# Kernel tuning notes

Hardware: AMD Instinct MI355X
Metric: run time of the kernel (lower is better)

Reference implementation:

```python
import jax, jax.numpy as jnp
import numpy as np

B, S, D = 4, 2048, 512
H, DK, DV = 8, 64, 64


def setup_inputs() -> dict:
    key = jax.random.key(0)
    ks = jax.random.split(key, 12)
    inv = 1.0 / np.sqrt(D)
    return {
        "query": jax.random.normal(ks[0], (B, S, D), dtype=jnp.float32),
        "value": jax.random.normal(ks[1], (B, S, D), dtype=jnp.float32),
        "attention_mask": jax.random.randint(ks[2], (B, S), 0, 2, dtype=jnp.int32),
        "Wq": jax.random.normal(ks[3], (D, H * DK), dtype=jnp.float32) * inv,
        "bq": jnp.zeros((H * DK,), dtype=jnp.float32),
        "Wk": jax.random.normal(ks[4], (D, H * DK), dtype=jnp.float32) * inv,
        "bk": jnp.zeros((H * DK,), dtype=jnp.float32),
        "Wv": jax.random.normal(ks[5], (D, H * DV), dtype=jnp.float32) * inv,
        "bv": jnp.zeros((H * DV,), dtype=jnp.float32),
        "Wo": jax.random.normal(ks[6], (H * DV, D), dtype=jnp.float32) * inv,
        "bo": jnp.zeros((D,), dtype=jnp.float32),
    }


def _split_heads(x, h):
    b, s, _ = x.shape
    return x.reshape(b, s, h, -1).transpose(0, 2, 1, 3)  # (B,H,S,dh)


def reference(query, value, attention_mask, Wq, bq, Wk, bk, Wv, bv, Wo, bo):
    # QKV projections (activation=None -> identity); key defaults to value
    q = _split_heads(query @ Wq + bq, H)   # (B,H,S,DK)
    k = _split_heads(value @ Wk + bk, H)   # (B,H,S,DK)
    v = _split_heads(value @ Wv + bv, H)   # (B,H,S,DV)

    scores = jnp.einsum("bhqd,bhkd->bhqk", q, k) / jnp.sqrt(jnp.float32(DK))
    # additive mask: m = 1e9*(mask-1), applied on both key and query axes
    m = 1e9 * (attention_mask.astype(jnp.float32) - 1.0)  # (B,S)
    scores = scores + m[:, None, None, :] + m[:, None, :, None]

    weights = jax.nn.softmax(scores, axis=-1)
    ctx = jnp.einsum("bhqk,bhkd->bhqd", weights, v)        # (B,H,S,DV)
    ctx = ctx.transpose(0, 2, 1, 3).reshape(ctx.shape[0], ctx.shape[2], H * DV)
    return ctx @ Wo + bo  # (B,S,D)
```

## Files before the change

### kernel.cpp

```cpp
#include <hip/hip_runtime.h>

#define B_ 4
#define S_ 2048
#define D_ 512
#define H_ 8

typedef __attribute__((ext_vector_type(8))) __bf16 bf16x8;
typedef __attribute__((ext_vector_type(4))) float f32x4;

#define NEGBIG  -1.442695040e9f
#define QSCALE  0.18033688011112042f

__device__ __forceinline__ unsigned pack_rn(float a, float b) {
    union { float f; unsigned u; } ua, ub; ua.f = a; ub.f = b;
    return __builtin_amdgcn_perm(ub.u + 0x8000u, ua.u + 0x8000u, 0x07060302u);
}

__global__ __launch_bounds__(256) void cast_x(
    const float* __restrict__ q, const float* __restrict__ v,
    unsigned short* __restrict__ xq, unsigned short* __restrict__ xv)
{
    const float* src = blockIdx.z ? v : q;
    unsigned short* dst = blockIdx.z ? xv : xq;
    int i = (blockIdx.x * 256 + threadIdx.x) * 8;
    float4 f0 = *(const float4*)&src[i];
    float4 f1 = *(const float4*)&src[i + 4];
    uint4 o;
    o.x = pack_rn(f0.x, f0.y); o.y = pack_rn(f0.z, f0.w);
    o.z = pack_rn(f1.x, f1.y); o.w = pack_rn(f1.z, f1.w);
    *(uint4*)&dst[i] = o;
}

__global__ __launch_bounds__(256) void cast_wt(
    const float* __restrict__ Wq, const float* __restrict__ Wk,
    const float* __restrict__ Wv, const float* __restrict__ Wo,
    unsigned short* __restrict__ Tq, unsigned short* __restrict__ Tk,
    unsigned short* __restrict__ Tv, unsigned short* __restrict__ To)
{
    int z = blockIdx.z;
    const float* W = (z == 0) ? Wq : (z == 1) ? Wk : (z == 2) ? Wv : Wo;
    unsigned short* T = (z == 0) ? Tq : (z == 1) ? Tk : (z == 2) ? Tv : To;
    int n0 = blockIdx.x * 64, k0 = blockIdx.y * 64;
    int tid = threadIdx.x;

    __shared__ float Ts[64][69];
    #pragma unroll
    for (int it = 0; it < 4; it++) {
        int lin = tid + it * 256;
        int kr = lin >> 4, c4 = (lin & 15) * 4;
        float4 v = *(const float4*)&W[(k0 + kr) * 512 + n0 + c4];
        Ts[kr][c4 + 0] = v.x; Ts[kr][c4 + 1] = v.y;
        Ts[kr][c4 + 2] = v.z; Ts[kr][c4 + 3] = v.w;
    }
    __syncthreads();
    int n = tid >> 2, kc = tid & 3;
    unsigned p[8];
    #pragma unroll
    for (int j = 0; j < 8; j++)
        p[j] = pack_rn(Ts[kc * 16 + 2 * j][n], Ts[kc * 16 + 2 * j + 1][n]);
    unsigned short* dst = &T[(n0 + n) * 512 + k0 + kc * 16];
    *(uint4*)dst       = *(uint4*)&p[0];
    *(uint4*)(dst + 8) = *(uint4*)&p[4];
}

__global__ __launch_bounds__(256) void proj_qkv_mfma(
    const unsigned short* __restrict__ Xq, const unsigned short* __restrict__ Xv,
    const unsigned short* __restrict__ Wtq, const unsigned short* __restrict__ Wtk,
    const unsigned short* __restrict__ Wtv,
    const float* __restrict__ bq, const float* __restrict__ bk,
    const float* __restrict__ bv,
    unsigned short* __restrict__ Qb, unsigned short* __restrict__ Kb,
    unsigned short* __restrict__ VtG)
{
    const int z = blockIdx.z;
    const unsigned short* A  = (z == 0) ? Wtq : (z == 1) ? Wtk : Xv;
    const unsigned short* Bm = (z == 0) ? Xq  : (z == 1) ? Xv  : Wtv;
    const float* bias        = (z == 0) ? bq  : (z == 1) ? bk  : bv;
    const int m0 = (z < 2) ? blockIdx.y * 128 : blockIdx.x * 128;
    const int n0 = (z < 2) ? blockIdx.x * 128 : blockIdx.y * 128;

    const int tid = threadIdx.x;
    const int w = tid >> 6, lane = tid & 63;
    const int l15 = lane & 15, quad = lane >> 4;
    const int wm = (w >> 1) * 64, wn = (w & 1) * 64;

    __shared__ unsigned short As[128 * 72];
    __shared__ unsigned short Bs[128 * 72];

    f32x4 acc[4][4];
    #pragma unroll
    for (int i = 0; i < 4; i++)
        #pragma unroll
        for (int j = 0; j < 4; j++) acc[i][j] = (f32x4){0.f, 0.f, 0.f, 0.f};

    for (int k0 = 0; k0 < 512; k0 += 64) {
        __syncthreads();
        #pragma unroll
        for (int it = 0; it < 2; it++) {
            int lin = tid + it * 256;
            int row = lin >> 2, c2 = (lin & 3) * 2;
            *(uint4*)&As[row * 72 + c2 * 8]     = *(const uint4*)&A[(m0 + row) * 512 + k0 + c2 * 8];
            *(uint4*)&As[row * 72 + c2 * 8 + 8] = *(const uint4*)&A[(m0 + row) * 512 + k0 + c2 * 8 + 8];
            *(uint4*)&Bs[row * 72 + c2 * 8]     = *(const uint4*)&Bm[(n0 + row) * 512 + k0 + c2 * 8];
            *(uint4*)&Bs[row * 72 + c2 * 8 + 8] = *(const uint4*)&Bm[(n0 + row) * 512 + k0 + c2 * 8 + 8];
        }
        __syncthreads();
        #pragma unroll
        for (int kc = 0; kc < 2; kc++) {
            bf16x8 a[4], bb[4];
            #pragma unroll
            for (int i = 0; i < 4; i++)
                a[i] = *(const bf16x8*)&As[(wm + 16 * i + l15) * 72 + kc * 32 + quad * 8];
            #pragma unroll
            for (int j = 0; j < 4; j++)
                bb[j] = *(const bf16x8*)&Bs[(wn + 16 * j + l15) * 72 + kc * 32 + quad * 8];
            #pragma unroll
            for (int i = 0; i < 4; i++)
                #pragma unroll
                for (int j = 0; j < 4; j++)
                    acc[i][j] = __builtin_amdgcn_mfma_f32_16x16x32_bf16(a[i], bb[j], acc[i][j], 0, 0, 0);
        }
    }

    if (z == 2) {
        #pragma unroll
        for (int j = 0; j < 4; j++) {
            int N = n0 + wn + 16 * j + l15;
            float bv_ = bias[N];
            int h = N >> 6, d = N & 63;
            #pragma unroll
            for (int i = 0; i < 4; i++) {
                int Mb = m0 + wm + 16 * i + quad * 4;
                int b = Mb >> 11, s = Mb & 2047;
                uint2 o;
                o.x = pack_rn(acc[i][j][0] + bv_, acc[i][j][1] + bv_);
                o.y = pack_rn(acc[i][j][2] + bv_, acc[i][j][3] + bv_);
                *(uint2*)&VtG[((b * H_ + h) * 64 + d) * 2048 + s] = o;
            }
        }
    } else {
        unsigned short* dst = (z == 0) ? Qb : Kb;
        const float scale = (z == 0) ? QSCALE : 1.0f;
        #pragma unroll
        for (int j = 0; j < 4; j++) {
            int sg = n0 + wn + 16 * j + l15;
            int b = sg >> 11, s = sg & 2047;
            #pragma unroll
            for (int i = 0; i < 4; i++) {
                int F = m0 + wm + 16 * i + quad * 4;
                int h = F >> 6, d = F & 63;
                float4 b4 = *(const float4*)&bias[F];
                uint2 o;
                o.x = pack_rn((acc[i][j][0] + b4.x) * scale, (acc[i][j][1] + b4.y) * scale);
                o.y = pack_rn((acc[i][j][2] + b4.z) * scale, (acc[i][j][3] + b4.w) * scale);
                *(uint2*)&dst[((b * H_ + h) * 2048 + s) * 64 + d] = o;
            }
        }
    }
}

__global__ __launch_bounds__(256) void flash_mfma(
    const unsigned short* __restrict__ Qg, const unsigned short* __restrict__ Kg,
    const unsigned short* __restrict__ VtG, const int* __restrict__ amask,
    unsigned short* __restrict__ ctxB)
{
    const int bh = blockIdx.y, b = bh >> 3, h = bh & 7;
    const int q0 = blockIdx.x * 128;
    const int tid = threadIdx.x;
    const int w = tid >> 6, lane = tid & 63;
    const int l15 = lane & 15, quad = lane >> 4;

    __shared__ unsigned short Ks[2][64 * 72];
    __shared__ unsigned short Ps[4][32 * 72];
    __shared__ float Km[4][64];

    const int* amask_b = amask + b * 2048;
    unsigned short* pw = &Ps[w][0];

    bf16x8 qf[2][2];
    float mq[2];
    #pragma unroll
    for (int qb = 0; qb < 2; qb++) {
        int qrow = q0 + w * 32 + qb * 16 + l15;
        const unsigned short* p = &Qg[(bh * 2048 + qrow) * 64 + quad * 8];
        qf[qb][0] = *(const bf16x8*)p;
        qf[qb][1] = *(const bf16x8*)(p + 32);
        mq[qb] = amask_b[qrow] ? 0.f : NEGBIG;
    }

    const int srow = tid >> 2;
    const int sch  = (tid & 3) * 2;
    const unsigned short* kgb = Kg + (long)bh * 2048 * 64;

    {
        uint4 k0a = *(const uint4*)&kgb[srow * 64 + sch * 8];
        uint4 k0b = *(const uint4*)&kgb[srow * 64 + sch * 8 + 8];
        *(uint4*)&Ks[0][srow * 72 + sch * 8]     = k0a;
        *(uint4*)&Ks[0][srow * 72 + sch * 8 + 8] = k0b;
    }
    int mreg = amask_b[lane];

    f32x4 accO[2][4];
    #pragma unroll
    for (int qb = 0; qb < 2; qb++)
        #pragma unroll
        for (int dt = 0; dt < 4; dt++) accO[qb][dt] = (f32x4){0.f, 0.f, 0.f, 0.f};
    float mi[2] = {-3.0e38f, -3.0e38f};
    float li[2] = {0.f, 0.f};

    __syncthreads();

    for (int t = 0; t < 32; t++) {
        const int kt = t * 64;
        const int ktn = (t < 31) ? kt + 64 : kt;
        const int cur = t & 1, nxt = cur ^ 1;

        bf16x8 vf[4][2];
        #pragma unroll
        for (int dt = 0; dt < 4; dt++)
            #pragma unroll
            for (int kc = 0; kc < 2; kc++)
                vf[dt][kc] = *(const bf16x8*)&VtG[(bh * 64 + dt * 16 + l15) * 2048 + kt + kc * 32 + quad * 8];
        uint4 kst0 = *(const uint4*)&kgb[(ktn + srow) * 64 + sch * 8];
        uint4 kst1 = *(const uint4*)&kgb[(ktn + srow) * 64 + sch * 8 + 8];
        Km[w][lane] = mreg ? 0.f : NEGBIG;
        mreg = amask_b[ktn + lane];

        f32x4 kmf[4];
        #pragma unroll
        for (int nt = 0; nt < 4; nt++)
            kmf[nt] = *(const f32x4*)&Km[w][nt * 16 + quad * 4];

        bf16x8 kf[4][2];
        #pragma unroll
        for (int nt = 0; nt < 4; nt++)
            #pragma unroll
            for (int kc = 0; kc < 2; kc++)
                kf[nt][kc] = *(const bf16x8*)&Ks[cur][(nt * 16 + l15) * 72 + kc * 32 + quad * 8];
        f32x4 sc[2][4];
        #pragma unroll
        for (int qb = 0; qb < 2; qb++)
            #pragma unroll
            for (int nt = 0; nt < 4; nt++) {
                sc[qb][nt] = kmf[nt] + mq[qb];
                #pragma unroll
                for (int kc = 0; kc < 2; kc++)
                    sc[qb][nt] = __builtin_amdgcn_mfma_f32_16x16x32_bf16(
                        kf[nt][kc], qf[qb][kc], sc[qb][nt], 0, 0, 0);
            }

        #pragma unroll
        for (int qb = 0; qb < 2; qb++) {
            float mloc = sc[qb][0][0];
            #pragma unroll
            for (int nt = 0; nt < 4; nt++)
                #pragma unroll
                for (int r = 0; r < 4; r++)
                    mloc = fmaxf(mloc, sc[qb][nt][r]);
            mloc = fmaxf(mloc, __shfl_xor(mloc, 16));
            mloc = fmaxf(mloc, __shfl_xor(mloc, 32));
            float mn = fmaxf(mi[qb], mloc);
            float alpha = __builtin_amdgcn_exp2f(mi[qb] - mn);
            float ps = 0.f;
            #pragma unroll
            for (int nt = 0; nt < 4; nt++) {
                float p0 = __builtin_amdgcn_exp2f(sc[qb][nt][0] - mn);
                float p1 = __builtin_amdgcn_exp2f(sc[qb][nt][1] - mn);
                float p2 = __builtin_amdgcn_exp2f(sc[qb][nt][2] - mn);
                float p3 = __builtin_amdgcn_exp2f(sc[qb][nt][3] - mn);
                ps += (p0 + p1) + (p2 + p3);
                int prow = (qb * 16 + l15) * 72 + nt * 16 + quad * 4;
                *(unsigned*)&pw[prow]     = pack_rn(p0, p1);
                *(unsigned*)&pw[prow + 2] = pack_rn(p2, p3);
            }
            ps += __shfl_xor(ps, 16);
            ps += __shfl_xor(ps, 32);
            li[qb] = li[qb] * alpha + ps;
            mi[qb] = mn;
            #pragma unroll
            for (int dt = 0; dt < 4; dt++) {
                accO[qb][dt][0] *= alpha; accO[qb][dt][1] *= alpha;
                accO[qb][dt][2] *= alpha; accO[qb][dt][3] *= alpha;
            }
        }

        #pragma unroll
        for (int qb = 0; qb < 2; qb++) {
            bf16x8 pf0 = *(const bf16x8*)&pw[(qb * 16 + l15) * 72 + quad * 8];
            bf16x8 pf1 = *(const bf16x8*)&pw[(qb * 16 + l15) * 72 + 32 + quad * 8];
            #pragma unroll
            for (int dt = 0; dt < 4; dt++) {
                accO[qb][dt] = __builtin_amdgcn_mfma_f32_16x16x32_bf16(
                    vf[dt][0], pf0, accO[qb][dt], 0, 0, 0);
                accO[qb][dt] = __builtin_amdgcn_mfma_f32_16x16x32_bf16(
                    vf[dt][1], pf1, accO[qb][dt], 0, 0, 0);
            }
        }

        *(uint4*)&Ks[nxt][srow * 72 + sch * 8]     = kst0;
        *(uint4*)&Ks[nxt][srow * 72 + sch * 8 + 8] = kst1;
        __syncthreads();
    }

    #pragma unroll
    for (int qb = 0; qb < 2; qb++) {
        float inv = 1.f / li[qb];
        int q = q0 + w * 32 + qb * 16 + l15;
        int obase = (b * 2048 + q) * 512 + h * 64 + quad * 4;
        #pragma unroll
        for (int dt = 0; dt < 4; dt++) {
            uint2 o;
            o.x = pack_rn(accO[qb][dt][0] * inv, accO[qb][dt][1] * inv);
            o.y = pack_rn(accO[qb][dt][2] * inv, accO[qb][dt][3] * inv);
            *(uint2*)&ctxB[obase + dt * 16] = o;
        }
    }
}

__global__ __launch_bounds__(256) void proj_out_mfma(
    const unsigned short* __restrict__ ctxB, const unsigned short* __restrict__ Wto,
    const float* __restrict__ bo, float* __restrict__ out)
{
    const int m0 = blockIdx.y * 128, n0 = blockIdx.x * 128;
    const int tid = threadIdx.x;
    const int w = tid >> 6, lane = tid & 63;
    const int l15 = lane & 15, quad = lane >> 4;
    const int wm = (w >> 1) * 64, wn = (w & 1) * 64;

    __shared__ unsigned short As[128 * 72];
    __shared__ unsigned short Bs[128 * 72];

    f32x4 acc[4][4];
    #pragma unroll
    for (int i = 0; i < 4; i++)
        #pragma unroll
        for (int j = 0; j < 4; j++) acc[i][j] = (f32x4){0.f, 0.f, 0.f, 0.f};

    for (int k0 = 0; k0 < 512; k0 += 64) {
        __syncthreads();
        #pragma unroll
        for (int it = 0; it < 2; it++) {
            int lin = tid + it * 256;
            int row = lin >> 2, c2 = (lin & 3) * 2;
            *(uint4*)&As[row * 72 + c2 * 8]     = *(const uint4*)&Wto[(m0 + row) * 512 + k0 + c2 * 8];
            *(uint4*)&As[row * 72 + c2 * 8 + 8] = *(const uint4*)&Wto[(m0 + row) * 512 + k0 + c2 * 8 + 8];
            *(uint4*)&Bs[row * 72 + c2 * 8]     = *(const uint4*)&ctxB[(n0 + row) * 512 + k0 + c2 * 8];
            *(uint4*)&Bs[row * 72 + c2 * 8 + 8] = *(const uint4*)&ctxB[(n0 + row) * 512 + k0 + c2 * 8 + 8];
        }
        __syncthreads();
        #pragma unroll
        for (int kc = 0; kc < 2; kc++) {
            bf16x8 a[4], bb[4];
            #pragma unroll
            for (int i = 0; i < 4; i++)
                a[i] = *(const bf16x8*)&As[(wm + 16 * i + l15) * 72 + kc * 32 + quad * 8];
            #pragma unroll
            for (int j = 0; j < 4; j++)
                bb[j] = *(const bf16x8*)&Bs[(wn + 16 * j + l15) * 72 + kc * 32 + quad * 8];
            #pragma unroll
            for (int i = 0; i < 4; i++)
                #pragma unroll
                for (int j = 0; j < 4; j++)
                    acc[i][j] = __builtin_amdgcn_mfma_f32_16x16x32_bf16(a[i], bb[j], acc[i][j], 0, 0, 0);
        }
    }

    #pragma unroll
    for (int j = 0; j < 4; j++) {
        int sg = n0 + wn + 16 * j + l15;
        #pragma unroll
        for (int i = 0; i < 4; i++) {
            int F = m0 + wm + 16 * i + quad * 4;
            float4 b4 = *(const float4*)&bo[F];
            float4 vv;
            vv.x = acc[i][j][0] + b4.x;
            vv.y = acc[i][j][1] + b4.y;
            vv.z = acc[i][j][2] + b4.z;
            vv.w = acc[i][j][3] + b4.w;
            *(float4*)&out[sg * 512 + F] = vv;
        }
    }
}

extern "C" void kernel_launch(void* const* d_in, const int* in_sizes, int n_in,
                              void* d_out, int out_size, void* d_ws, size_t ws_size,
                              hipStream_t stream)
{
    const float* query = (const float*)d_in[0];
    const float* value = (const float*)d_in[1];
    const int*   amask = (const int*)d_in[2];
    const float* Wq = (const float*)d_in[3];
    const float* bq = (const float*)d_in[4];
    const float* Wk = (const float*)d_in[5];
    const float* bk = (const float*)d_in[6];
    const float* Wv = (const float*)d_in[7];
    const float* bv = (const float*)d_in[8];
    const float* Wo = (const float*)d_in[9];
    const float* bo = (const float*)d_in[10];
    float* out = (float*)d_out;

    char* ws = (char*)d_ws;
    const size_t MB = 1 << 20;
    unsigned short* Xbq = (unsigned short*)(ws);
    unsigned short* Xbv = (unsigned short*)(ws + 8 * MB);
    unsigned short* Wtq = (unsigned short*)(ws + 16 * MB);
    unsigned short* Wtk = (unsigned short*)(ws + 16 * MB + MB / 2);
    unsigned short* Wtv = (unsigned short*)(ws + 17 * MB);
    unsigned short* Wto = (unsigned short*)(ws + 17 * MB + MB / 2);
    unsigned short* Qb  = (unsigned short*)(ws + 18 * MB);
    unsigned short* Kb  = (unsigned short*)(ws + 26 * MB);
    unsigned short* VtG = (unsigned short*)(ws + 34 * MB);
    unsigned short* ctx = (unsigned short*)(ws + 42 * MB);

    cast_x<<<dim3(2048, 1, 2), 256, 0, stream>>>(query, value, Xbq, Xbv);
    cast_wt<<<dim3(8, 8, 4), 256, 0, stream>>>(Wq, Wk, Wv, Wo, Wtq, Wtk, Wtv, Wto);
    proj_qkv_mfma<<<dim3(64, 4, 3), 256, 0, stream>>>(Xbq, Xbv, Wtq, Wtk, Wtv,
                                                      bq, bk, bv, Qb, Kb, VtG);
    flash_mfma<<<dim3(16, 32), 256, 0, stream>>>(Qb, Kb, VtG, amask, ctx);
    proj_out_mfma<<<dim3(64, 4), 256, 0, stream>>>(ctx, Wto, bo, out);
}
```

Baseline: 214.8 us.

## Halve flash query tile and stage V tiles through double-buffered LDS

The flash attention kernel now gives each block 64 query rows instead of 128, with one 16-row block per wave, and doubles the grid to 1024 blocks with a launch bound asking for 4 blocks per CU. V tiles are now loaded cooperatively into a double-buffered shared-memory buffer alongside K, where before each wave read them directly from global memory into registers. The aim is more blocks and lower register pressure for better latency hiding, plus coalesced V loads. The cost is that every K/V tile is now fetched twice as often across the grid, and each wave does less MFMA work per tile load and barrier.

```diff
diff --git a/kernel.cpp b/kernel.cpp
--- a/kernel.cpp
+++ b/kernel.cpp
@@ -159,54 +159,50 @@
     }
 }
 
-__global__ __launch_bounds__(256) void flash_mfma(
+__global__ __launch_bounds__(256, 4) void flash_mfma(
     const unsigned short* __restrict__ Qg, const unsigned short* __restrict__ Kg,
     const unsigned short* __restrict__ VtG, const int* __restrict__ amask,
     unsigned short* __restrict__ ctxB)
 {
     const int bh = blockIdx.y, b = bh >> 3, h = bh & 7;
-    const int q0 = blockIdx.x * 128;
+    const int q0 = blockIdx.x * 64;
     const int tid = threadIdx.x;
     const int w = tid >> 6, lane = tid & 63;
     const int l15 = lane & 15, quad = lane >> 4;
 
     __shared__ unsigned short Ks[2][64 * 72];
-    __shared__ unsigned short Ps[4][32 * 72];
+    __shared__ unsigned short Vs[2][64 * 72];
+    __shared__ unsigned short Ps[4][16 * 72];
     __shared__ float Km[4][64];
 
     const int* amask_b = amask + b * 2048;
     unsigned short* pw = &Ps[w][0];
 
-    bf16x8 qf[2][2];
-    float mq[2];
-    #pragma unroll
-    for (int qb = 0; qb < 2; qb++) {
-        int qrow = q0 + w * 32 + qb * 16 + l15;
+    const int qrow = q0 + w * 16 + l15;
+    bf16x8 qf[2];
+    {
         const unsigned short* p = &Qg[(bh * 2048 + qrow) * 64 + quad * 8];
-        qf[qb][0] = *(const bf16x8*)p;
-        qf[qb][1] = *(const bf16x8*)(p + 32);
-        mq[qb] = amask_b[qrow] ? 0.f : NEGBIG;
-    }
+        qf[0] = *(const bf16x8*)p;
+        qf[1] = *(const bf16x8*)(p + 32);
+    }
+    const float mq = amask_b[qrow] ? 0.f : NEGBIG;
 
     const int srow = tid >> 2;
     const int sch  = (tid & 3) * 2;
-    const unsigned short* kgb = Kg + (long)bh * 2048 * 64;
-
-    {
-        uint4 k0a = *(const uint4*)&kgb[srow * 64 + sch * 8];
-        uint4 k0b = *(const uint4*)&kgb[srow * 64 + sch * 8 + 8];
-        *(uint4*)&Ks[0][srow * 72 + sch * 8]     = k0a;
-        *(uint4*)&Ks[0][srow * 72 + sch * 8 + 8] = k0b;
-    }
+    const unsigned short* kgb = Kg  + (long)bh * 2048 * 64;
+    const unsigned short* vgb = VtG + (long)bh * 64 * 2048;
+
+    *(uint4*)&Ks[0][srow * 72 + sch * 8]     = *(const uint4*)&kgb[srow * 64 + sch * 8];
+    *(uint4*)&Ks[0][srow * 72 + sch * 8 + 8] = *(const uint4*)&kgb[srow * 64 + sch * 8 + 8];
+    *(uint4*)&Vs[0][srow * 72 + sch * 8]     = *(const uint4*)&vgb[srow * 2048 + sch * 8];
+    *(uint4*)&Vs[0][srow * 72 + sch * 8 + 8] = *(const uint4*)&vgb[srow * 2048 + sch * 8 + 8];
     int mreg = amask_b[lane];
 
-    f32x4 accO[2][4];
-    #pragma unroll
-    for (int qb = 0; qb < 2; qb++)
-        #pragma unroll
-        for (int dt = 0; dt < 4; dt++) accO[qb][dt] = (f32x4){0.f, 0.f, 0.f, 0.f};
-    float mi[2] = {-3.0e38f, -3.0e38f};
-    float li[2] = {0.f, 0.f};
+    f32x4 accO[4];
+    #pragma unroll
+    for (int dt = 0; dt < 4; dt++) accO[dt] = (f32x4){0.f, 0.f, 0.f, 0.f};
+    float mi = -3.0e38f;
+    float li = 0.f;
 
     __syncthreads();
 
@@ -215,14 +211,10 @@
         const int ktn = (t < 31) ? kt + 64 : kt;
         const int cur = t & 1, nxt = cur ^ 1;
 
-        bf16x8 vf[4][2];
-        #pragma unroll
-        for (int dt = 0; dt < 4; dt++)
-            #pragma unroll
-            for (int kc = 0; kc < 2; kc++)
-                vf[dt][kc] = *(const bf16x8*)&VtG[(bh * 64 + dt * 16 + l15) * 2048 + kt + kc * 32 + quad * 8];
-        uint4 kst0 = *(const uint4*)&kgb[(ktn + srow) * 64 + sch * 8];
-        uint4 kst1 = *(const uint4*)&kgb[(ktn + srow) * 64 + sch * 8 + 8];
+        uint4 ka0 = *(const uint4*)&kgb[(ktn + srow) * 64 + sch * 8];
+        uint4 ka1 = *(const uint4*)&kgb[(ktn + srow) * 64 + sch * 8 + 8];
+        uint4 va0 = *(const uint4*)&vgb[srow * 2048 + ktn + sch * 8];
+        uint4 va1 = *(const uint4*)&vgb[srow * 2048 + ktn + sch * 8 + 8];
         Km[w][lane] = mreg ? 0.f : NEGBIG;
         mreg = amask_b[ktn + lane];
 
@@ -231,89 +223,78 @@
         for (int nt = 0; nt < 4; nt++)
             kmf[nt] = *(const f32x4*)&Km[w][nt * 16 + quad * 4];
 
-        bf16x8 kf[4][2];
-        #pragma unroll
-        for (int nt = 0; nt < 4; nt++)
-            #pragma unroll
-            for (int kc = 0; kc < 2; kc++)
-                kf[nt][kc] = *(const bf16x8*)&Ks[cur][(nt * 16 + l15) * 72 + kc * 32 + quad * 8];
-        f32x4 sc[2][4];
-        #pragma unroll
-        for (int qb = 0; qb < 2; qb++)
-            #pragma unroll
-            for (int nt = 0; nt < 4; nt++) {
-                sc[qb][nt] = kmf[nt] + mq[qb];
-                #pragma unroll
-                for (int kc = 0; kc < 2; kc++)
-                    sc[qb][nt] = __builtin_amdgcn_mfma_f32_16x16x32_bf16(
-                        kf[nt][kc], qf[qb][kc], sc[qb][nt], 0, 0, 0);
-            }
-
-        #pragma unroll
-        for (int qb = 0; qb < 2; qb++) {
-            float mloc = sc[qb][0][0];
+        f32x4 sc[4];
+        #pragma unroll
+        for (int nt = 0; nt < 4; nt++) {
+            sc[nt] = kmf[nt] + mq;
+            #pragma unroll
+            for (int kc = 0; kc < 2; kc++) {
+                bf16x8 kf = *(const bf16x8*)&Ks[cur][(nt * 16 + l15) * 72 + kc * 32 + quad * 8];
+                sc[nt] = __builtin_amdgcn_mfma_f32_16x16x32_bf16(kf, qf[kc], sc[nt], 0, 0, 0);
+            }
+        }
+
+        {
+            float mloc = sc[0][0];
             #pragma unroll
             for (int nt = 0; nt < 4; nt++)
                 #pragma unroll
                 for (int r = 0; r < 4; r++)
-                    mloc = fmaxf(mloc, sc[qb][nt][r]);
+                    mloc = fmaxf(mloc, sc[nt][r]);
             mloc = fmaxf(mloc, __shfl_xor(mloc, 16));
             mloc = fmaxf(mloc, __shfl_xor(mloc, 32));
-            float mn = fmaxf(mi[qb], mloc);
-            float alpha = __builtin_amdgcn_exp2f(mi[qb] - mn);
+            float mn = fmaxf(mi, mloc);
+            float alpha = __builtin_amdgcn_exp2f(mi - mn);
             float ps = 0.f;
             #pragma unroll
             for (int nt = 0; nt < 4; nt++) {
-                float p0 = __builtin_amdgcn_exp2f(sc[qb][nt][0] - mn);
-                float p1 = __builtin_amdgcn_exp2f(sc[qb][nt][1] - mn);
-                float p2 = __builtin_amdgcn_exp2f(sc[qb][nt][2] - mn);
-                float p3 = __builtin_amdgcn_exp2f(sc[qb][nt][3] - mn);
+                float p0 = __builtin_amdgcn_exp2f(sc[nt][0] - mn);
+                float p1 = __builtin_amdgcn_exp2f(sc[nt][1] - mn);
+                float p2 = __builtin_amdgcn_exp2f(sc[nt][2] - mn);
+                float p3 = __builtin_amdgcn_exp2f(sc[nt][3] - mn);
                 ps += (p0 + p1) + (p2 + p3);
-                int prow = (qb * 16 + l15) * 72 + nt * 16 + quad * 4;
+                int prow = l15 * 72 + nt * 16 + quad * 4;
                 *(unsigned*)&pw[prow]     = pack_rn(p0, p1);
                 *(unsigned*)&pw[prow + 2] = pack_rn(p2, p3);
             }
             ps += __shfl_xor(ps, 16);
             ps += __shfl_xor(ps, 32);
-            li[qb] = li[qb] * alpha + ps;
-            mi[qb] = mn;
+            li = li * alpha + ps;
+            mi = mn;
             #pragma unroll
             for (int dt = 0; dt < 4; dt++) {
-                accO[qb][dt][0] *= alpha; accO[qb][dt][1] *= alpha;
-                accO[qb][dt][2] *= alpha; accO[qb][dt][3] *= alpha;
-            }
-        }
-
-        #pragma unroll
-        for (int qb = 0; qb < 2; qb++) {
-            bf16x8 pf0 = *(const bf16x8*)&pw[(qb * 16 + l15) * 72 + quad * 8];
-            bf16x8 pf1 = *(const bf16x8*)&pw[(qb * 16 + l15) * 72 + 32 + quad * 8];
+                accO[dt][0] *= alpha; accO[dt][1] *= alpha;
+                accO[dt][2] *= alpha; accO[dt][3] *= alpha;
+            }
+        }
+
+        {
+            bf16x8 pf0 = *(const bf16x8*)&pw[l15 * 72 + quad * 8];
+            bf16x8 pf1 = *(const bf16x8*)&pw[l15 * 72 + 32 + quad * 8];
             #pragma unroll
             for (int dt = 0; dt < 4; dt++) {
-                accO[qb][dt] = __builtin_amdgcn_mfma_f32_16x16x32_bf16(
-                    vf[dt][0], pf0, accO[qb][dt], 0, 0, 0);
-                accO[qb][dt] = __builtin_amdgcn_mfma_f32_16x16x32_bf16(
-                    vf[dt][1], pf1, accO[qb][dt], 0, 0, 0);
-            }
-        }
-
-        *(uint4*)&Ks[nxt][srow * 72 + sch * 8]     = kst0;
-        *(uint4*)&Ks[nxt][srow * 72 + sch * 8 + 8] = kst1;
+                bf16x8 vf0 = *(const bf16x8*)&Vs[cur][(dt * 16 + l15) * 72 + quad * 8];
+                bf16x8 vf1 = *(const bf16x8*)&Vs[cur][(dt * 16 + l15) * 72 + 32 + quad * 8];
+                accO[dt] = __builtin_amdgcn_mfma_f32_16x16x32_bf16(vf0, pf0, accO[dt], 0, 0, 0);
+                accO[dt] = __builtin_amdgcn_mfma_f32_16x16x32_bf16(vf1, pf1, accO[dt], 0, 0, 0);
+            }
+        }
+
+        *(uint4*)&Ks[nxt][srow * 72 + sch * 8]     = ka0;
+        *(uint4*)&Ks[nxt][srow * 72 + sch * 8 + 8] = ka1;
+        *(uint4*)&Vs[nxt][srow * 72 + sch * 8]     = va0;
+        *(uint4*)&Vs[nxt][srow * 72 + sch * 8 + 8] = va1;
         __syncthreads();
     }
 
-    #pragma unroll
-    for (int qb = 0; qb < 2; qb++) {
-        float inv = 1.f / li[qb];
-        int q = q0 + w * 32 + qb * 16 + l15;
-        int obase = (b * 2048 + q) * 512 + h * 64 + quad * 4;
-        #pragma unroll
-        for (int dt = 0; dt < 4; dt++) {
-            uint2 o;
-            o.x = pack_rn(accO[qb][dt][0] * inv, accO[qb][dt][1] * inv);
-            o.y = pack_rn(accO[qb][dt][2] * inv, accO[qb][dt][3] * inv);
-            *(uint2*)&ctxB[obase + dt * 16] = o;
-        }
+    const float inv = 1.f / li;
+    const int obase = (b * 2048 + qrow) * 512 + h * 64 + quad * 4;
+    #pragma unroll
+    for (int dt = 0; dt < 4; dt++) {
+        uint2 o;
+        o.x = pack_rn(accO[dt][0] * inv, accO[dt][1] * inv);
+        o.y = pack_rn(accO[dt][2] * inv, accO[dt][3] * inv);
+        *(uint2*)&ctxB[obase + dt * 16] = o;
     }
 }
 
@@ -416,6 +397,6 @@
     cast_wt<<<dim3(8, 8, 4), 256, 0, stream>>>(Wq, Wk, Wv, Wo, Wtq, Wtk, Wtv, Wto);
     proj_qkv_mfma<<<dim3(64, 4, 3), 256, 0, stream>>>(Xbq, Xbv, Wtq, Wtk, Wtv,
                                                       bq, bk, bv, Qb, Kb, VtG);
-    flash_mfma<<<dim3(16, 32), 256, 0, stream>>>(Qb, Kb, VtG, amask, ctx);
+    flash_mfma<<<dim3(32, 32), 256, 0, stream>>>(Qb, Kb, VtG, amask, ctx);
     proj_out_mfma<<<dim3(64, 4), 256, 0, stream>>>(ctx, Wto, bo, out);
 }
```

New measurement: 229.7 us. +6.9%, slower.
